# Optimization experiments

Hardware: AMD Instinct MI355X
Metric: run time of the kernel (lower is better)

The kernel has to match this reference:

```python
import jax, jax.numpy as jnp
import numpy as np

KAPPA = 5  # kNN neighbors per node (module hardcodes kappas = [5]*B, topk of KAPPA+2)


def build_graph(inputs):
    """Vectorized equivalent of get_graph(): returns flat (src, dst, edge_weight)
    over the B*S node space. Filtered kNN edges (dst < 2) are masked via weight 0,
    which is mathematically identical to removing them (gcn_norm uses edge weights)."""
    B, S, _ = inputs.shape
    diff = inputs[:, :, None, :] - inputs[:, None, :, :]            # [B,S,S,2]
    deltas = jnp.sqrt(jnp.sum(diff * diff, axis=-1))                # torch.cdist
    eye = jnp.eye(S, dtype=bool)
    d = jnp.where(eye[None], jnp.inf, deltas)                       # fill_diagonal_(inf)
    nodes = jnp.arange(2, S, dtype=jnp.int32)                       # non-depot nodes
    # depot edges: 0 -> i  and  i -> 1  for i in [2, S)
    src_dep = jnp.concatenate([jnp.zeros(S - 2, jnp.int32), nodes])
    dst_dep = jnp.concatenate([nodes, jnp.ones(S - 2, jnp.int32)])
    # kNN edges: 7 nearest per non-depot node (diag=inf so i never selected)
    _, idx = jax.lax.top_k(-d[:, 2:, :], KAPPA + 2)                 # [B, S-2, 7]
    src_knn = jnp.broadcast_to(nodes[:, None], (S - 2, KAPPA + 2)).reshape(-1)
    dst_knn = idx.reshape(B, -1).astype(jnp.int32)                  # [B, 7*(S-2)]
    mask_knn = (dst_knn >= 2).astype(jnp.float32)                   # drop depot dsts
    src = jnp.concatenate([jnp.broadcast_to(src_dep[None], (B, src_dep.shape[0])), jnp.broadcast_to(src_knn[None], (B, src_knn.shape[0]))], axis=1)
    dst = jnp.concatenate([jnp.broadcast_to(dst_dep[None], (B, dst_dep.shape[0])), dst_knn], axis=1)
    ew = jnp.concatenate([jnp.ones((B, dst_dep.shape[0]), jnp.float32), mask_knn], axis=1)
    offs = (jnp.arange(B, dtype=jnp.int32) * S)[:, None]            # batch node offset
    return (src + offs).reshape(-1), (dst + offs).reshape(-1), ew.reshape(-1)


def gcn_conv(x, src, dst, norm, self_norm, W, b, N):
    h = x @ W                                                       # GCNConv linear
    agg = jax.ops.segment_sum(h[src] * norm[:, None], dst, num_segments=N)
    agg = agg + h * self_norm[:, None]                              # self-loop term
    return agg + b


def gnn_forward(x, src, dst, ew, W0, b0, W1, b1, W2, b2):
    N = x.shape[0]
    deg = jax.ops.segment_sum(ew, dst, num_segments=N) + 1.0        # +1 self-loop
    dinv = 1.0 / jnp.sqrt(deg)
    norm = dinv[src] * dinv[dst] * ew                               # sym gcn_norm
    self_norm = dinv * dinv
    h = jax.nn.relu(gcn_conv(x, src, dst, norm, self_norm, W0, b0, N))
    h = jax.nn.relu(gcn_conv(h, src, dst, norm, self_norm, W1, b1, N))
    return gcn_conv(h, src, dst, norm, self_norm, W2, b2, N)


def setup_inputs() -> dict:
    B, S, D, H = 64, 1000, 128, 512
    key = jax.random.key(0)
    ks = jax.random.split(key, 12)
    sc = lambda fan_in: 1.0 / np.sqrt(fan_in)
    return {
        "inputs": jax.random.uniform(ks[0], (B, S, 2), jnp.float32),
        "scor": jax.random.uniform(ks[1], (B, S, 1), jnp.float32),
        "Wc": jax.random.normal(ks[2], (2, D), jnp.float32) * sc(2),
        "bc": jax.random.normal(ks[3], (D,), jnp.float32) * 0.01,
        "Ws": jax.random.normal(ks[4], (1, D), jnp.float32) * sc(1),
        "bs": jax.random.normal(ks[5], (D,), jnp.float32) * 0.01,
        "W0": jax.random.normal(ks[6], (D, H), jnp.float32) * sc(D),
        "b0": jnp.zeros((H,), jnp.float32),
        "W1": jax.random.normal(ks[8], (H, H), jnp.float32) * sc(H),
        "b1": jnp.zeros((H,), jnp.float32),
        "W2": jax.random.normal(ks[10], (H, D), jnp.float32) * sc(H),
        "b2": jnp.zeros((D,), jnp.float32),
    }


def reference(inputs, scor, Wc, bc, Ws, bs, W0, b0, W1, b1, W2, b2):
    B, S, _ = inputs.shape
    src, dst, ew = build_graph(inputs)
    x = (inputs @ Wc + bc) + (scor @ Ws + bs)                       # embedded_data
    x = x.reshape(B * S, -1)
    out = gnn_forward(x, src, dst, ew, W0, b0, W1, b1, W2, b2)
    return out.reshape(B, S, -1)
```

## Files before the change

kernel.cpp:

```cpp
#include <hip/hip_runtime.h>

typedef unsigned short u16;
typedef unsigned int u32;
typedef unsigned long long u64;
using short8 = __attribute__((ext_vector_type(8))) short;
using f32x4  = __attribute__((ext_vector_type(4))) float;

constexpr int Bb = 64, Ss = 1000, Dd = 128, Hh = 512;
constexpr int NN = Bb * Ss;
constexpr int NSRC = Ss - 2;

__device__ __forceinline__ float bf2f(u16 h) {
    u32 u = ((u32)h) << 16;
    return __builtin_bit_cast(float, u);
}
__device__ __forceinline__ u16 f2bf(float v) {
    u32 u = __builtin_bit_cast(u32, v);
    u32 r = (u + 0x7FFFu + ((u >> 16) & 1u)) >> 16;
    return (u16)r;
}
__device__ __forceinline__ float4 bf4(ushort4 v) {
    float4 r;
    r.x = bf2f(v.x); r.y = bf2f(v.y); r.z = bf2f(v.z); r.w = bf2f(v.w);
    return r;
}
__device__ __forceinline__ void gl_lds16(const void* g, void* l) {
    __builtin_amdgcn_global_load_lds(
        (const __attribute__((address_space(1))) void*)g,
        (__attribute__((address_space(3))) void*)l, 16, 0, 0);
}
__device__ __forceinline__ void acc8(float (&a)[8], uint4 v, float w) {
    u32 c[4] = {v.x, v.y, v.z, v.w};
#pragma unroll
    for (int k = 0; k < 4; ++k) {
        float lo = __builtin_bit_cast(float, c[k] << 16);
        float hi = __builtin_bit_cast(float, c[k] & 0xFFFF0000u);
        a[2 * k]     += lo * w;
        a[2 * k + 1] += hi * w;
    }
}
__device__ __forceinline__ void unp8(float (&a)[8], uint4 v) {
    u32 c[4] = {v.x, v.y, v.z, v.w};
#pragma unroll
    for (int k = 0; k < 4; ++k) {
        a[2 * k]     = __builtin_bit_cast(float, c[k] << 16);
        a[2 * k + 1] = __builtin_bit_cast(float, c[k] & 0xFFFF0000u);
    }
}

__device__ __forceinline__ u64 umin64(u64 a, u64 b) { return a < b ? a : b; }
__device__ __forceinline__ u64 umax64(u64 a, u64 b) { return a < b ? b : a; }

__device__ __forceinline__ void ins8u(u64 (&bd)[8], u64 v) {
#pragma unroll
    for (int k = 7; k >= 1; --k)
        bd[k] = umin64(umax64(v, bd[k - 1]), bd[k]);
    bd[0] = umin64(v, bd[0]);
}

__device__ __forceinline__ void merge8(u64 (&a)[8], int mask) {
    u64 b[8];
#pragma unroll
    for (int k = 0; k < 8; ++k)
        b[k] = __shfl_xor((unsigned long long)a[k], mask);
    u64 m[8];
#pragma unroll
    for (int k = 0; k < 8; ++k) m[k] = umin64(a[k], b[7 - k]);
#pragma unroll
    for (int k = 0; k < 4; ++k) {
        u64 lo = umin64(m[k], m[k + 4]), hi = umax64(m[k], m[k + 4]);
        m[k] = lo; m[k + 4] = hi;
    }
#pragma unroll
    for (int base = 0; base < 8; base += 4)
#pragma unroll
        for (int k = 0; k < 2; ++k) {
            u64 lo = umin64(m[base + k], m[base + k + 2]);
            u64 hi = umax64(m[base + k], m[base + k + 2]);
            m[base + k] = lo; m[base + k + 2] = hi;
        }
#pragma unroll
    for (int base = 0; base < 8; base += 2) {
        u64 lo = umin64(m[base], m[base + 1]), hi = umax64(m[base], m[base + 1]);
        m[base] = lo; m[base + 1] = hi;
    }
#pragma unroll
    for (int k = 0; k < 8; ++k) a[k] = m[k];
}

__global__ __launch_bounds__(256) void knn_bin_kernel(const float* __restrict__ inputs,
                                                      float2* __restrict__ gsxy,
                                                      u16* __restrict__ gsid,
                                                      int* __restrict__ gcst) {
    __shared__ float px[Ss], py[Ss];
    __shared__ int hist[256];
    __shared__ int cur[256];
    int b = blockIdx.x;
    int tid = threadIdx.x;
    const float* base = inputs + (size_t)b * Ss * 2;
    for (int t = tid; t < Ss; t += 256) { px[t] = base[2 * t]; py[t] = base[2 * t + 1]; }
    hist[tid] = 0;
    __syncthreads();
    for (int t = tid; t < Ss; t += 256) {
        int cx = min(15, (int)(px[t] * 16.0f));
        int cy = min(15, (int)(py[t] * 16.0f));
        atomicAdd(&hist[cy * 16 + cx], 1);
    }
    __syncthreads();
    int cnt = hist[tid];
    for (int s = 1; s < 256; s <<= 1) {
        int u = (tid >= s) ? hist[tid - s] : 0;
        __syncthreads();
        hist[tid] += u;
        __syncthreads();
    }
    int st = hist[tid] - cnt;
    cur[tid] = st;
    gcst[b * 260 + tid] = st;
    if (tid == 0) gcst[b * 260 + 256] = Ss;
    __syncthreads();
    for (int t = tid; t < Ss; t += 256) {
        float x = px[t], y = py[t];
        int cx = min(15, (int)(x * 16.0f));
        int cy = min(15, (int)(y * 16.0f));
        int p = atomicAdd(&cur[cy * 16 + cx], 1);
        gsxy[b * 1000 + p] = make_float2(x, y);
        gsid[b * 1000 + p] = (u16)t;
    }
}

__global__ __launch_bounds__(256) void knn_query_kernel(const float* __restrict__ inputs,
                                                        const float2* __restrict__ gsxy,
                                                        const u16* __restrict__ gsid,
                                                        const int* __restrict__ gcst,
                                                        u16* __restrict__ knn,
                                                        int* __restrict__ indeg) {
    __shared__ float2 sxy[Ss];
    __shared__ u16 sid[Ss];
    __shared__ int cst[257];
    int b = blockIdx.x;
    int tid = threadIdx.x;
    for (int t = tid; t < Ss; t += 256) { sxy[t] = gsxy[b * 1000 + t]; sid[t] = gsid[b * 1000 + t]; }
    for (int t = tid; t < 257; t += 256) cst[t] = gcst[b * 260 + t];
    __syncthreads();

    int sub = tid & 7;
    int g = tid >> 3;
    int i = 2 + blockIdx.y * 32 + g;
    if (i >= Ss) return;

    float x = inputs[(size_t)b * 2000 + 2 * i];
    float y = inputs[(size_t)b * 2000 + 2 * i + 1];
    int cx = min(15, (int)(x * 16.0f));
    int cy = min(15, (int)(y * 16.0f));
    const float INF = __builtin_inff();
    constexpr float h = 0.0625f;

    u64 bd[8];
    int w = 1;
    for (;;) {
#pragma unroll
        for (int k = 0; k < 8; ++k) bd[k] = ~0ULL;
        int x0 = max(0, cx - w), x1 = min(15, cx + w);
        int y0 = max(0, cy - w), y1 = min(15, cy + w);
        for (int cyy = y0; cyy <= y1; ++cyy) {
            int p0 = cst[cyy * 16 + x0];
            int p1 = cst[cyy * 16 + x1 + 1];
            for (int p = p0 + sub; p < p1; p += 8) {
                float2 q = sxy[p];
                int j = sid[p];
                float dx = __fsub_rn(x, q.x);
                float dy = __fsub_rn(y, q.y);
                float d2 = __fadd_rn(__fmul_rn(dx, dx), __fmul_rn(dy, dy));
                float d = __fsqrt_rn(d2);
                u64 key = (((u64)__builtin_bit_cast(u32, d)) << 32) | (u32)j;
                key = (j == i) ? ~0ULL : key;
                ins8u(bd, key);
            }
        }
        merge8(bd, 1); merge8(bd, 2); merge8(bd, 4);
        float d7 = __builtin_bit_cast(float, (u32)(bd[6] >> 32));
        float bL = (x0 > 0)  ? (x - (float)x0 * h) : INF;
        float bR = (x1 < 15) ? ((float)(x1 + 1) * h - x) : INF;
        float bB = (y0 > 0)  ? (y - (float)y0 * h) : INF;
        float bT = (y1 < 15) ? ((float)(y1 + 1) * h - y) : INF;
        float bound = fminf(fminf(bL, bR), fminf(bB, bT));
        if (d7 <= bound - 2e-6f || w >= 16) break;
        ++w;
    }

    if (sub == 0) {
        u16* kp = knn + ((size_t)b * NSRC + (i - 2)) * 7;
#pragma unroll
        for (int k = 0; k < 7; ++k) {
            int j = (int)(u32)bd[k];
            kp[k] = (u16)j;
            if (j >= 2) atomicAdd(&indeg[b * Ss + j], 1);
        }
    }
}

__global__ void deg_dinv_kernel(const int* __restrict__ indeg, float* __restrict__ dinv) {
    int n = blockIdx.x * 256 + threadIdx.x;
    if (n >= NN) return;
    int i = n % Ss;
    float deg = (i == 0) ? 1.0f : (i == 1) ? (float)(Ss - 1) : (float)(indeg[n] + 2);
    dinv[n] = 1.0f / __fsqrt_rn(deg);
}

__global__ __launch_bounds__(1024) void scan1_kernel(const int* __restrict__ indeg,
                                                     int* __restrict__ offs,
                                                     int* __restrict__ bsum) {
    __shared__ int sh[1024];
    int t = threadIdx.x;
    int idx = blockIdx.x * 1024 + t;
    int v = (idx < NN) ? indeg[idx] : 0;
    sh[t] = v;
    __syncthreads();
    for (int off = 1; off < 1024; off <<= 1) {
        int u = (t >= off) ? sh[t - off] : 0;
        __syncthreads();
        sh[t] += u;
        __syncthreads();
    }
    if (idx < NN) offs[idx] = sh[t] - v;
    if (t == 1023) bsum[blockIdx.x] = sh[1023];
}

__global__ void scan2_kernel(int* __restrict__ bsum) {
    if (threadIdx.x == 0) {
        int run = 0;
        for (int k = 0; k < 63; ++k) { int v = bsum[k]; bsum[k] = run; run += v; }
        bsum[63] = run;
    }
}

__global__ __launch_bounds__(1024) void scan3_kernel(int* __restrict__ offs,
                                                     const int* __restrict__ bsum) {
    int idx = blockIdx.x * 1024 + threadIdx.x;
    if (idx < NN) offs[idx] += bsum[blockIdx.x];
    if (idx == 0) offs[NN] = bsum[63];
}

__global__ __launch_bounds__(256) void fill_rev_kernel(const u16* __restrict__ knn,
                                                       const int* __restrict__ offs,
                                                       int* __restrict__ cursor,
                                                       u16* __restrict__ rev) {
    if (threadIdx.x >= 250) return;
    int b = blockIdx.x;
    int i = 2 + blockIdx.y * 250 + threadIdx.x;
    if (i >= Ss) return;
    const u16* kp = knn + ((size_t)b * NSRC + (i - 2)) * 7;
#pragma unroll
    for (int k = 0; k < 7; ++k) {
        int d = kp[k];
        if (d >= 2) {
            int n = b * Ss + d;
            int p = atomicAdd(&cursor[n], 1);
            rev[offs[n] + p] = (u16)i;
        }
    }
}

__global__ __launch_bounds__(512) void fuse0_kernel(const float* __restrict__ Wc,
                                                    const float* __restrict__ bc,
                                                    const float* __restrict__ Ws,
                                                    const float* __restrict__ bs,
                                                    const float* __restrict__ W0,
                                                    float* __restrict__ A) {
    int h = threadIdx.x;
    float a0 = 0.f, a1 = 0.f, a2 = 0.f, a3 = 0.f;
    for (int c = 0; c < Dd; ++c) {
        float w = W0[c * Hh + h];
        a0 += Wc[c] * w;
        a1 += Wc[Dd + c] * w;
        a2 += Ws[c] * w;
        a3 += (bc[c] + bs[c]) * w;
    }
    A[h] = a0; A[Hh + h] = a1; A[2 * Hh + h] = a2; A[3 * Hh + h] = a3;
}

__global__ __launch_bounds__(1024) void agg_e_kernel(const float* __restrict__ inputs,
                                                     const float* __restrict__ scor,
                                                     const float* __restrict__ dinv,
                                                     const int* __restrict__ offs,
                                                     const int* __restrict__ indeg,
                                                     const u16* __restrict__ rev,
                                                     float4* __restrict__ ve) {
    __shared__ float se0[Ss], se1[Ss], se2[Ss], sdv[Ss];
    __shared__ float4 depw[16];
    int b = blockIdx.x;
    int tid = threadIdx.x;
    int nb = b * Ss;
    const float* base = inputs + (size_t)nb * 2;
    for (int t = tid; t < Ss; t += 1024) {
        se0[t] = base[2 * t];
        se1[t] = base[2 * t + 1];
        se2[t] = scor[nb + t];
        sdv[t] = dinv[nb + t];
    }
    __syncthreads();

    float4 dep = {0.f, 0.f, 0.f, 0.f};
    for (int r = tid; r < Ss; r += 1024) {
        if (r >= 2) {
            float w = sdv[r];
            dep.x += se0[r] * w; dep.y += se1[r] * w;
            dep.z += se2[r] * w; dep.w += w;
        }
    }
#pragma unroll
    for (int m = 1; m < 64; m <<= 1) {
        dep.x += __shfl_xor(dep.x, m);
        dep.y += __shfl_xor(dep.y, m);
        dep.z += __shfl_xor(dep.z, m);
        dep.w += __shfl_xor(dep.w, m);
    }
    if ((tid & 63) == 0) depw[tid >> 6] = dep;
    __syncthreads();

    int i = tid;
    if (i >= Ss) return;
    float dn = sdv[i], sn = dn * dn;
    float4 acc = {0.f, 0.f, 0.f, 0.f};
    if (i >= 2) {
        int n = nb + i;
        int cnt = indeg[n], o = offs[n];
        float w0 = sdv[0];
        acc.x = se0[0] * w0; acc.y = se1[0] * w0;
        acc.z = se2[0] * w0; acc.w = w0;
        for (int e = 0; e < cnt; ++e) {
            int s = rev[o + e];
            float w = sdv[s];
            acc.x += se0[s] * w; acc.y += se1[s] * w;
            acc.z += se2[s] * w; acc.w += w;
        }
    } else if (i == 1) {
        float4 t = {0.f, 0.f, 0.f, 0.f};
#pragma unroll
        for (int k = 0; k < 16; ++k) {
            t.x += depw[k].x; t.y += depw[k].y;
            t.z += depw[k].z; t.w += depw[k].w;
        }
        acc = t;
    }
    float4 v;
    v.x = acc.x * dn + se0[i] * sn;
    v.y = acc.y * dn + se1[i] * sn;
    v.z = acc.z * dn + se2[i] * sn;
    v.w = acc.w * dn + sn;
    ve[nb + i] = v;
}

__global__ __launch_bounds__(256) void expand512_kernel(const float4* __restrict__ ve,
                                                        const float* __restrict__ A,
                                                        const float* __restrict__ bias,
                                                        u16* __restrict__ X) {
    int gid = blockIdx.x * 256 + threadIdx.x;
    if (gid >= NN * 128) return;
    int n = gid >> 7, t = gid & 127;
    int h = t * 4;
    float4 v = ve[n];
    float4 a0 = *(const float4*)(A + h);
    float4 a1 = *(const float4*)(A + Hh + h);
    float4 a2 = *(const float4*)(A + 2 * Hh + h);
    float4 a3 = *(const float4*)(A + 3 * Hh + h);
    float4 bz = *(const float4*)(bias + h);
    ushort4 o;
    o.x = f2bf(fmaxf(v.x * a0.x + v.y * a1.x + v.z * a2.x + v.w * a3.x + bz.x, 0.f));
    o.y = f2bf(fmaxf(v.x * a0.y + v.y * a1.y + v.z * a2.y + v.w * a3.y + bz.y, 0.f));
    o.z = f2bf(fmaxf(v.x * a0.z + v.y * a1.z + v.z * a2.z + v.w * a3.z + bz.z, 0.f));
    o.w = f2bf(fmaxf(v.x * a0.w + v.y * a1.w + v.z * a2.w + v.w * a3.w + bz.w, 0.f));
    *(ushort4*)(X + (size_t)n * Hh + h) = o;
}

__global__ void transp_kernel(const float* __restrict__ src,
                              u16* __restrict__ dst, int R, int C) {
    int gid = blockIdx.x * 256 + threadIdx.x;
    if (gid >= R * C) return;
    int r = gid / C, c = gid - r * C;
    dst[c * R + r] = f2bf(src[gid]);
}

__global__ __launch_bounds__(256) void gemm_kernel(const u16* __restrict__ A,
                                                   const u16* __restrict__ W,
                                                   u16* __restrict__ Y,
                                                   int K, int Ncols,
                                                   int nyb, int nxb) {
    __shared__ __align__(16) u16 lA[128][64];
    __shared__ __align__(16) u16 lW[128][64];

    int grp = blockIdx.x / (8 * nxb);
    int rem = blockIdx.x - grp * (8 * nxb);
    int xcd = rem & 7;
    int xb  = rem >> 3;
    int yb  = grp * 8 + xcd;
    if (yb >= nyb) return;

    int row0 = yb * 128;
    int col0 = xb * 128;
    int tid = threadIdx.x;
    int lane = tid & 63, wid = tid >> 6;
    int wm = (wid >> 1) * 64, wn = (wid & 1) * 64;
    int lanelo = lane & 15, quad = lane >> 4;

    int lrow = lane >> 3;
    int lslot = lane & 7;

    f32x4 acc[4][4] = {};

    for (int k0 = 0; k0 < K; k0 += 64) {
#pragma unroll
        for (int t = 0; t < 4; ++t) {
            int chunk = t * 4 + wid;
            int row = chunk * 8 + lrow;
            int sc = lslot ^ (row & 7);
            gl_lds16(A + (size_t)(row0 + row) * K + k0 + sc * 8, &lA[chunk * 8][0]);
        }
#pragma unroll
        for (int t = 0; t < 4; ++t) {
            int chunk = t * 4 + wid;
            int row = chunk * 8 + lrow;
            int sc = lslot ^ (row & 7);
            gl_lds16(W + (size_t)(col0 + row) * K + k0 + sc * 8, &lW[chunk * 8][0]);
        }
        __syncthreads();

#pragma unroll
        for (int kk = 0; kk < 64; kk += 32) {
            short8 af[4], bw[4];
            int cbb = (kk >> 3) + quad;
#pragma unroll
            for (int mt = 0; mt < 4; ++mt) {
                int r = wm + mt * 16 + lanelo;
                af[mt] = *(const short8*)&lA[r][((cbb ^ (r & 7))) * 8];
            }
#pragma unroll
            for (int nt = 0; nt < 4; ++nt) {
                int r = wn + nt * 16 + lanelo;
                bw[nt] = *(const short8*)&lW[r][((cbb ^ (r & 7))) * 8];
            }
#pragma unroll
            for (int mt = 0; mt < 4; ++mt)
#pragma unroll
                for (int nt = 0; nt < 4; ++nt)
                    acc[mt][nt] = __builtin_amdgcn_mfma_f32_16x16x32_bf16(
                        af[mt], bw[nt], acc[mt][nt], 0, 0, 0);
        }
        __syncthreads();
    }

#pragma unroll
    for (int mt = 0; mt < 4; ++mt)
#pragma unroll
        for (int nt = 0; nt < 4; ++nt)
#pragma unroll
            for (int r = 0; r < 4; ++r) {
                int row = row0 + wm + mt * 16 + quad * 4 + r;
                int col = col0 + wn + nt * 16 + lanelo;
                Y[(size_t)row * Ncols + col] = f2bf(acc[mt][nt][r]);
            }
}

__global__ __launch_bounds__(1024) void dep1_kernel(const u16* __restrict__ y,
                                                    const float* __restrict__ dinv,
                                                    float* __restrict__ dq,
                                                    int M) {
    int b = blockIdx.x;
    int qq = blockIdx.y;
    int co = blockIdx.z * 128;
    int tid = threadIdx.x;
    int c4 = tid & 31;
    int es = tid >> 5;
    int j0 = 2 + qq * 250;
    int j1 = j0 + 250; if (j1 > Ss) j1 = Ss;
    const u16* yb = y + (size_t)b * Ss * M + co + c4 * 4;
    const float* dv = dinv + b * Ss;
    float a0 = 0.f, a1 = 0.f, a2 = 0.f, a3 = 0.f;
    for (int j = j0 + es; j < j1; j += 32) {
        float w = dv[j];
        float4 u = bf4(*(const ushort4*)(yb + (size_t)j * M));
        a0 += u.x * w; a1 += u.y * w; a2 += u.z * w; a3 += u.w * w;
    }
    __shared__ float4 red[1024];
    float4 mv; mv.x = a0; mv.y = a1; mv.z = a2; mv.w = a3;
    red[tid] = mv;
    __syncthreads();
#pragma unroll
    for (int s = 16; s > 0; s >>= 1) {
        if (es < s) {
            float4 o = red[tid + (s << 5)];
            float4 m = red[tid];
            m.x += o.x; m.y += o.y; m.z += o.z; m.w += o.w;
            red[tid] = m;
        }
        __syncthreads();
    }
    if (es == 0)
        *(float4*)(dq + ((size_t)qq * Bb + b) * M + co + c4 * 4) = red[c4];
}

__global__ __launch_bounds__(256) void aggw512_kernel(const u16* __restrict__ y,
                                                      const float* __restrict__ dinv,
                                                      const int* __restrict__ offs,
                                                      const int* __restrict__ indeg,
                                                      const u16* __restrict__ rev,
                                                      const float* __restrict__ bias,
                                                      const float* __restrict__ dep1,
                                                      u16* __restrict__ oX) {
    int tid = threadIdx.x;
    int wv = tid >> 6, lane = tid & 63;
    int bx = blockIdx.x;
    int b = (bx & 7) + 8 * (bx / 2000);
    int i = ((bx >> 3) % 250) * 4 + wv;
    int nb = b * Ss;
    int n = nb + i;
    const u16* yB = y + (size_t)nb * 512 + lane * 8;

    float acc[8] = {};
    if (i >= 2) {
        int cnt = indeg[n], o = offs[n];
        int rv = 0; float rw = 0.f;
        if (lane < 16 && lane < cnt) { rv = rev[o + lane]; rw = dinv[nb + rv]; }
        float w0 = dinv[nb];
        uint4 v0 = *(const uint4*)yB;
        acc8(acc, v0, w0);
        int cl = cnt < 16 ? cnt : 16;
        int e = 0;
        for (; e + 4 <= cl; e += 4) {
            int   s0 = __shfl(rv, e),     s1 = __shfl(rv, e + 1);
            int   s2 = __shfl(rv, e + 2), s3 = __shfl(rv, e + 3);
            float w_0 = __shfl(rw, e),     w_1 = __shfl(rw, e + 1);
            float w_2 = __shfl(rw, e + 2), w_3 = __shfl(rw, e + 3);
            uint4 u0 = *(const uint4*)(yB + (size_t)s0 * 512);
            uint4 u1 = *(const uint4*)(yB + (size_t)s1 * 512);
            uint4 u2 = *(const uint4*)(yB + (size_t)s2 * 512);
            uint4 u3 = *(const uint4*)(yB + (size_t)s3 * 512);
            acc8(acc, u0, w_0); acc8(acc, u1, w_1);
            acc8(acc, u2, w_2); acc8(acc, u3, w_3);
        }
        for (; e < cl; ++e) {
            int s = __shfl(rv, e); float ww = __shfl(rw, e);
            uint4 u = *(const uint4*)(yB + (size_t)s * 512);
            acc8(acc, u, ww);
        }
        for (; e < cnt; ++e) {
            int s = rev[o + e]; float ww = dinv[nb + s];
            uint4 u = *(const uint4*)(yB + (size_t)s * 512);
            acc8(acc, u, ww);
        }
    } else if (i == 1) {
        const float* dp = dep1 + (size_t)b * 512 + lane * 8;
#pragma unroll
        for (int qq = 0; qq < 4; ++qq) {
            float4 v0 = *(const float4*)(dp + (size_t)qq * Bb * 512);
            float4 v1 = *(const float4*)(dp + (size_t)qq * Bb * 512 + 4);
            acc[0] += v0.x; acc[1] += v0.y; acc[2] += v0.z; acc[3] += v0.w;
            acc[4] += v1.x; acc[5] += v1.y; acc[6] += v1.z; acc[7] += v1.w;
        }
    }
    float dn = dinv[n], sn = dn * dn;
    float s8[8];
    unp8(s8, *(const uint4*)(yB + (size_t)i * 512));
    float4 bl = *(const float4*)(bias + lane * 8);
    float4 bh = *(const float4*)(bias + lane * 8 + 4);
    float bz[8] = {bl.x, bl.y, bl.z, bl.w, bh.x, bh.y, bh.z, bh.w};
    u32 ow[4];
#pragma unroll
    for (int k = 0; k < 4; ++k) {
        float z0 = acc[2 * k]     * dn + s8[2 * k]     * sn + bz[2 * k];
        float z1 = acc[2 * k + 1] * dn + s8[2 * k + 1] * sn + bz[2 * k + 1];
        ow[k] = (u32)f2bf(fmaxf(z0, 0.f)) | ((u32)f2bf(fmaxf(z1, 0.f)) << 16);
    }
    uint4 ov = {ow[0], ow[1], ow[2], ow[3]};
    *(uint4*)(oX + (size_t)n * 512 + lane * 8) = ov;
}

__global__ __launch_bounds__(128) void agg128f_kernel(const u16* __restrict__ y,
                                                      const float* __restrict__ dinv,
                                                      const int* __restrict__ offs,
                                                      const int* __restrict__ indeg,
                                                      const u16* __restrict__ rev,
                                                      const float* __restrict__ bias,
                                                      const float* __restrict__ dep1,
                                                      float* __restrict__ out) {
    int bx = blockIdx.x;
    int x = bx & 7, q = bx >> 3;
    int bb = q / 1000;
    int i = q - bb * 1000;
    int b = x + (bb << 3);
    int n = b * Ss + i;
    int nb = n - i;
    int tid = threadIdx.x, c = tid;

    __shared__ int   sidx[128];
    __shared__ float sw[128];
    int cnt = 0, o = 0;
    if (i >= 2) { cnt = indeg[n]; o = offs[n]; }
    int cl = cnt < 128 ? cnt : 128;
    if (tid < cl) {
        int s = rev[o + tid];
        sidx[tid] = s;
        sw[tid] = dinv[nb + s];
    }
    __syncthreads();

    float a = 0.f;
    if (i >= 2) {
        a = bf2f(y[(size_t)nb * 128 + c]) * dinv[nb];
        int e = 0;
        for (; e + 4 <= cl; e += 4) {
            int s0 = sidx[e], s1 = sidx[e + 1], s2 = sidx[e + 2], s3 = sidx[e + 3];
            float w0 = sw[e], w1 = sw[e + 1], w2 = sw[e + 2], w3 = sw[e + 3];
            float u0 = bf2f(y[(size_t)(nb + s0) * 128 + c]);
            float u1 = bf2f(y[(size_t)(nb + s1) * 128 + c]);
            float u2 = bf2f(y[(size_t)(nb + s2) * 128 + c]);
            float u3 = bf2f(y[(size_t)(nb + s3) * 128 + c]);
            a += u0 * w0 + u1 * w1 + u2 * w2 + u3 * w3;
        }
        for (; e < cl; ++e) a += bf2f(y[(size_t)(nb + sidx[e]) * 128 + c]) * sw[e];
        for (int e2 = 128; e2 < cnt; ++e2) {
            int s = rev[o + e2];
            a += bf2f(y[(size_t)(nb + s) * 128 + c]) * dinv[nb + s];
        }
    } else if (i == 1) {
#pragma unroll
        for (int qq = 0; qq < 4; ++qq)
            a += dep1[((size_t)qq * Bb + b) * 128 + c];
    }
    float dn = dinv[n];
    out[(size_t)n * 128 + c] = a * dn + bf2f(y[(size_t)n * 128 + c]) * (dn * dn) + bias[c];
}

constexpr size_t O_INDEG  = 0;
constexpr size_t O_CURSOR = 256000;
constexpr size_t O_OFFS   = 512000;
constexpr size_t O_DINV   = 768256;
constexpr size_t O_KNN    = 1024256;
constexpr size_t O_REV    = 1918080;
constexpr size_t O_AMAT   = 2811904;
constexpr size_t O_WT1    = 2942976;
constexpr size_t O_WT2    = 3467264;
constexpr size_t O_X      = 3598336;
constexpr size_t O_Y      = 69134336;
constexpr size_t O_DEP1A  = 134670336;
constexpr size_t O_DEP1B  = 135194624;
constexpr size_t O_BSUM   = 135325696;
constexpr size_t O_GSXY   = O_X;
constexpr size_t O_GSID   = O_X + 512000;
constexpr size_t O_GCST   = O_X + 640000;
constexpr size_t O_VE     = O_Y;

extern "C" void kernel_launch(void* const* d_in, const int* in_sizes, int n_in,
                              void* d_out, int out_size, void* d_ws, size_t ws_size,
                              hipStream_t stream) {
    const float* inputs = (const float*)d_in[0];
    const float* scor   = (const float*)d_in[1];
    const float* Wc     = (const float*)d_in[2];
    const float* bc     = (const float*)d_in[3];
    const float* Ws     = (const float*)d_in[4];
    const float* bs     = (const float*)d_in[5];
    const float* W0     = (const float*)d_in[6];
    const float* b0     = (const float*)d_in[7];
    const float* W1     = (const float*)d_in[8];
    const float* b1     = (const float*)d_in[9];
    const float* W2     = (const float*)d_in[10];
    const float* b2     = (const float*)d_in[11];

    char* w = (char*)d_ws;
    int*    indeg  = (int*)(w + O_INDEG);
    int*    cursor = (int*)(w + O_CURSOR);
    int*    offs   = (int*)(w + O_OFFS);
    float*  dinv   = (float*)(w + O_DINV);
    u16*    knn    = (u16*)(w + O_KNN);
    u16*    rev    = (u16*)(w + O_REV);
    float*  amat   = (float*)(w + O_AMAT);
    u16*    wt1    = (u16*)(w + O_WT1);
    u16*    wt2    = (u16*)(w + O_WT2);
    u16*    xbf    = (u16*)(w + O_X);
    u16*    ybf    = (u16*)(w + O_Y);
    float*  dep1a  = (float*)(w + O_DEP1A);
    float*  dep1b  = (float*)(w + O_DEP1B);
    int*    bsum   = (int*)(w + O_BSUM);
    float2* gsxy   = (float2*)(w + O_GSXY);
    u16*    gsid   = (u16*)(w + O_GSID);
    int*    gcst   = (int*)(w + O_GCST);
    float4* ve     = (float4*)(w + O_VE);

    hipMemsetAsync(w + O_INDEG, 0, 512000, stream);

    knn_bin_kernel<<<Bb, 256, 0, stream>>>(inputs, gsxy, gsid, gcst);
    knn_query_kernel<<<dim3(Bb, 32), 256, 0, stream>>>(inputs, gsxy, gsid, gcst, knn, indeg);
    deg_dinv_kernel<<<250, 256, 0, stream>>>(indeg, dinv);
    scan1_kernel<<<63, 1024, 0, stream>>>(indeg, offs, bsum);
    scan2_kernel<<<1, 64, 0, stream>>>(bsum);
    scan3_kernel<<<63, 1024, 0, stream>>>(offs, bsum);
    fill_rev_kernel<<<dim3(Bb, 4), 256, 0, stream>>>(knn, offs, cursor, rev);

    fuse0_kernel<<<1, 512, 0, stream>>>(Wc, bc, Ws, bs, W0, amat);
    transp_kernel<<<(Hh * Hh + 255) / 256, 256, 0, stream>>>(W1, wt1, Hh, Hh);
    transp_kernel<<<(Hh * Dd + 255) / 256, 256, 0, stream>>>(W2, wt2, Hh, Dd);

    agg_e_kernel<<<Bb, 1024, 0, stream>>>(inputs, scor, dinv, offs, indeg, rev, ve);
    expand512_kernel<<<NN * 128 / 256, 256, 0, stream>>>(ve, amat, b0, xbf);
    gemm_kernel<<<63 * 32, 256, 0, stream>>>(xbf, wt1, ybf, Hh, Hh, 500, 4);
    dep1_kernel<<<dim3(Bb, 4, 4), 1024, 0, stream>>>(ybf, dinv, dep1a, Hh);
    aggw512_kernel<<<NN / 4, 256, 0, stream>>>(ybf, dinv, offs, indeg, rev, b1, dep1a, xbf);
    gemm_kernel<<<63 * 8, 256, 0, stream>>>(xbf, wt2, ybf, Hh, Dd, 500, 1);
    dep1_kernel<<<dim3(Bb, 4, 1), 1024, 0, stream>>>(ybf, dinv, dep1b, Dd);
    agg128f_kernel<<<NN, 128, 0, stream>>>(ybf, dinv, offs, indeg, rev, b2, dep1b, (float*)d_out);
}
```

Measured before the change: 338.5 us.

## Fuse depot-sink column reduction into GEMM epilogue with atomics

Drops the separate dep1 reduction kernels. The GEMM epilogue now accumulates the dinv-weighted column sums of the freshly produced Y tile per batch, reduces across lanes with shuffles, and atomically adds them into a zeroed per-batch buffer. The aggregation kernels read one fused value instead of four partials. This removes two launches and a re-read of Y, at the cost of extra epilogue work, global float atomics, non-deterministic summation order, and a new memset.

```diff
diff --git a/kernel.cpp b/kernel.cpp
--- a/kernel.cpp
+++ b/kernel.cpp
@@ -385,6 +385,8 @@
 __global__ __launch_bounds__(256) void gemm_kernel(const u16* __restrict__ A,
                                                    const u16* __restrict__ W,
                                                    u16* __restrict__ Y,
+                                                   const float* __restrict__ dinv,
+                                                   float* __restrict__ dep,
                                                    int K, int Ncols,
                                                    int nyb, int nxb) {
     __shared__ __align__(16) u16 lA[128][64];
@@ -450,54 +452,33 @@
         __syncthreads();
     }
 
-#pragma unroll
-    for (int mt = 0; mt < 4; ++mt)
-#pragma unroll
-        for (int nt = 0; nt < 4; ++nt)
+    int bA = row0 / 1000;
+    int boundary = (bA + 1) * 1000;
+#pragma unroll
+    for (int nt = 0; nt < 4; ++nt) {
+        float d0 = 0.f, d1 = 0.f;
+#pragma unroll
+        for (int mt = 0; mt < 4; ++mt)
 #pragma unroll
             for (int r = 0; r < 4; ++r) {
                 int row = row0 + wm + mt * 16 + quad * 4 + r;
                 int col = col0 + wn + nt * 16 + lanelo;
-                Y[(size_t)row * Ncols + col] = f2bf(acc[mt][nt][r]);
+                u16 hv = f2bf(acc[mt][nt][r]);
+                Y[(size_t)row * Ncols + col] = hv;
+                int bb = (row >= boundary) ? bA + 1 : bA;
+                int ii = row - bb * 1000;
+                float wgt = (ii >= 2) ? dinv[row] : 0.f;
+                float v = bf2f(hv) * wgt;
+                if (row >= boundary) d1 += v; else d0 += v;
             }
-}
-
-__global__ __launch_bounds__(1024) void dep1_kernel(const u16* __restrict__ y,
-                                                    const float* __restrict__ dinv,
-                                                    float* __restrict__ dq,
-                                                    int M) {
-    int b = blockIdx.x;
-    int qq = blockIdx.y;
-    int co = blockIdx.z * 128;
-    int tid = threadIdx.x;
-    int c4 = tid & 31;
-    int es = tid >> 5;
-    int j0 = 2 + qq * 250;
-    int j1 = j0 + 250; if (j1 > Ss) j1 = Ss;
-    const u16* yb = y + (size_t)b * Ss * M + co + c4 * 4;
-    const float* dv = dinv + b * Ss;
-    float a0 = 0.f, a1 = 0.f, a2 = 0.f, a3 = 0.f;
-    for (int j = j0 + es; j < j1; j += 32) {
-        float w = dv[j];
-        float4 u = bf4(*(const ushort4*)(yb + (size_t)j * M));
-        a0 += u.x * w; a1 += u.y * w; a2 += u.z * w; a3 += u.w * w;
-    }
-    __shared__ float4 red[1024];
-    float4 mv; mv.x = a0; mv.y = a1; mv.z = a2; mv.w = a3;
-    red[tid] = mv;
-    __syncthreads();
-#pragma unroll
-    for (int s = 16; s > 0; s >>= 1) {
-        if (es < s) {
-            float4 o = red[tid + (s << 5)];
-            float4 m = red[tid];
-            m.x += o.x; m.y += o.y; m.z += o.z; m.w += o.w;
-            red[tid] = m;
-        }
-        __syncthreads();
-    }
-    if (es == 0)
-        *(float4*)(dq + ((size_t)qq * Bb + b) * M + co + c4 * 4) = red[c4];
+        d0 += __shfl_xor(d0, 16); d0 += __shfl_xor(d0, 32);
+        d1 += __shfl_xor(d1, 16); d1 += __shfl_xor(d1, 32);
+        if (quad == 0) {
+            int col = col0 + wn + nt * 16 + lanelo;
+            if (d0 != 0.f) atomicAdd(&dep[bA * Ncols + col], d0);
+            if (d1 != 0.f) atomicAdd(&dep[(bA + 1) * Ncols + col], d1);
+        }
+    }
 }
 
 __global__ __launch_bounds__(256) void aggw512_kernel(const u16* __restrict__ y,
@@ -551,13 +532,10 @@
         }
     } else if (i == 1) {
         const float* dp = dep1 + (size_t)b * 512 + lane * 8;
-#pragma unroll
-        for (int qq = 0; qq < 4; ++qq) {
-            float4 v0 = *(const float4*)(dp + (size_t)qq * Bb * 512);
-            float4 v1 = *(const float4*)(dp + (size_t)qq * Bb * 512 + 4);
-            acc[0] += v0.x; acc[1] += v0.y; acc[2] += v0.z; acc[3] += v0.w;
-            acc[4] += v1.x; acc[5] += v1.y; acc[6] += v1.z; acc[7] += v1.w;
-        }
+        float4 v0 = *(const float4*)dp;
+        float4 v1 = *(const float4*)(dp + 4);
+        acc[0] = v0.x; acc[1] = v0.y; acc[2] = v0.z; acc[3] = v0.w;
+        acc[4] = v1.x; acc[5] = v1.y; acc[6] = v1.z; acc[7] = v1.w;
     }
     float dn = dinv[n], sn = dn * dn;
     float s8[8];
@@ -624,9 +602,7 @@
             a += bf2f(y[(size_t)(nb + s) * 128 + c]) * dinv[nb + s];
         }
     } else if (i == 1) {
-#pragma unroll
-        for (int qq = 0; qq < 4; ++qq)
-            a += dep1[((size_t)qq * Bb + b) * 128 + c];
+        a = dep1[(size_t)b * 128 + c];
     }
     float dn = dinv[n];
     out[(size_t)n * 128 + c] = a * dn + bf2f(y[(size_t)n * 128 + c]) * (dn * dn) + bias[c];
@@ -644,7 +620,7 @@
 constexpr size_t O_X      = 3598336;
 constexpr size_t O_Y      = 69134336;
 constexpr size_t O_DEP1A  = 134670336;
-constexpr size_t O_DEP1B  = 135194624;
+constexpr size_t O_DEP1B  = 134801408;
 constexpr size_t O_BSUM   = 135325696;
 constexpr size_t O_GSXY   = O_X;
 constexpr size_t O_GSID   = O_X + 512000;
@@ -688,6 +664,7 @@
     float4* ve     = (float4*)(w + O_VE);
 
     hipMemsetAsync(w + O_INDEG, 0, 512000, stream);
+    hipMemsetAsync(w + O_DEP1A, 0, 131072 + 32768, stream);
 
     knn_bin_kernel<<<Bb, 256, 0, stream>>>(inputs, gsxy, gsid, gcst);
     knn_query_kernel<<<dim3(Bb, 32), 256, 0, stream>>>(inputs, gsxy, gsid, gcst, knn, indeg);
@@ -703,10 +680,8 @@
 
     agg_e_kernel<<<Bb, 1024, 0, stream>>>(inputs, scor, dinv, offs, indeg, rev, ve);
     expand512_kernel<<<NN * 128 / 256, 256, 0, stream>>>(ve, amat, b0, xbf);
-    gemm_kernel<<<63 * 32, 256, 0, stream>>>(xbf, wt1, ybf, Hh, Hh, 500, 4);
-    dep1_kernel<<<dim3(Bb, 4, 4), 1024, 0, stream>>>(ybf, dinv, dep1a, Hh);
+    gemm_kernel<<<63 * 32, 256, 0, stream>>>(xbf, wt1, ybf, dinv, dep1a, Hh, Hh, 500, 4);
     aggw512_kernel<<<NN / 4, 256, 0, stream>>>(ybf, dinv, offs, indeg, rev, b1, dep1a, xbf);
-    gemm_kernel<<<63 * 8, 256, 0, stream>>>(xbf, wt2, ybf, Hh, Dd, 500, 1);
-    dep1_kernel<<<dim3(Bb, 4, 1), 1024, 0, stream>>>(ybf, dinv, dep1b, Dd);
+    gemm_kernel<<<63 * 8, 256, 0, stream>>>(xbf, wt2, ybf, dinv, dep1b, Hh, Dd, 500, 1);
     agg128f_kernel<<<NN, 128, 0, stream>>>(ybf, dinv, offs, indeg, rev, b2, dep1b, (float*)d_out);
 }
```

After: 346.7 us. 1.02x slower.
